# Kernel tuning notes

Hardware: AMD Instinct MI355X
Metric: run time of the kernel (lower is better)

## Reference

```python
import jax, jax.numpy as jnp
import numpy as np
import math

N = 50000      # nodes
E = 800000     # edges
IN = 256       # in_dim
HD = 128       # n_hid
T = 3          # num_types
R = 4          # num_relations
NH = 8         # n_heads
DK = HD // NH  # d_k = 16
L = 2          # n_layers
MAXT = 240     # RTE max_len


def _rte_table():
    # Faithful to the torch code (including its precedence: (10000**arange)/n_hid/2,
    # which overflows to inf for large indices -> div_term -> 0).
    pos = jnp.arange(MAXT, dtype=jnp.float32)[:, None]
    div = 1.0 / (10000.0 ** jnp.arange(0.0, HD * 2, 2.0, dtype=jnp.float32) / HD / 2.0)
    emb = jnp.zeros((MAXT, HD * 2), jnp.float32)
    emb = emb.at[:, 0::2].set(jnp.sin(pos * div) / math.sqrt(HD))
    emb = emb.at[:, 1::2].set(jnp.cos(pos * div) / math.sqrt(HD))
    return emb


def setup_inputs() -> dict:
    key = jax.random.key(0)
    ks = jax.random.split(key, 20)
    s = 0.02
    inp = {}
    inp["node_feature"] = jax.random.normal(ks[0], (N, IN), jnp.float32)
    inp["node_type"] = jax.random.randint(ks[1], (N,), 0, T)
    inp["edge_time"] = jax.random.randint(ks[2], (E,), 0, MAXT)
    inp["edge_type"] = jax.random.randint(ks[3], (E,), 0, R)
    inp["edge_index"] = jax.random.randint(ks[4], (2, E), 0, N)
    # adapt layer (per node type)
    inp["adapt_W"] = jax.random.normal(ks[5], (T, IN, HD), jnp.float32) * s
    inp["adapt_b"] = jax.random.normal(ks[6], (T, HD), jnp.float32) * s
    # per-layer, per-type linears (stored as [in,out] so y = x @ W + b)
    inp["Wk"] = jax.random.normal(ks[7], (L, T, HD, HD), jnp.float32) * s
    inp["bk"] = jnp.zeros((L, T, HD), jnp.float32)
    inp["Wq"] = jax.random.normal(ks[8], (L, T, HD, HD), jnp.float32) * s
    inp["bq"] = jnp.zeros((L, T, HD), jnp.float32)
    inp["Wv"] = jax.random.normal(ks[9], (L, T, HD, HD), jnp.float32) * s
    inp["bv"] = jnp.zeros((L, T, HD), jnp.float32)
    inp["Wa"] = jax.random.normal(ks[10], (L, T, HD, HD), jnp.float32) * s
    inp["ba"] = jnp.zeros((L, T, HD), jnp.float32)
    inp["rel_pri"] = jnp.ones((L, T, R, T, NH), jnp.float32)
    glorot = math.sqrt(6.0 / (DK + DK))
    inp["rel_att"] = jax.random.uniform(ks[11], (L, R, NH, DK, DK), jnp.float32, -glorot, glorot)
    inp["rel_msg"] = jax.random.uniform(ks[12], (L, R, NH, DK, DK), jnp.float32, -glorot, glorot)
    inp["skip"] = jnp.ones((L, T), jnp.float32)
    inp["rte_emb"] = _rte_table()                                   # [240, 2*HD], frozen sinusoid
    inp["rte_W"] = jax.random.normal(ks[13], (L, HD * 2, HD), jnp.float32) * s
    inp["rte_b"] = jnp.zeros((L, HD), jnp.float32)
    return inp


def _per_type_linear(x, types, W, b):
    # x:[M,in], types:[M] in [0,T); W:[T,in,out], b:[T,out]
    out = jnp.zeros((x.shape[0], W.shape[-1]), x.dtype)
    for t in range(W.shape[0]):
        out = jnp.where((types == t)[:, None], x @ W[t] + b[t], out)
    return out


def _segment_softmax(s, seg, n):
    # s:[E,H] softmax over edges sharing the same target node
    m = jax.ops.segment_max(s, seg, num_segments=n)
    e = jnp.exp(s - m[seg])
    z = jax.ops.segment_sum(e, seg, num_segments=n)
    return e / z[seg]


def _forward(node_feature, node_type, edge_time, edge_type, edge_index,
             adapt_W, adapt_b, Wk, bk, Wq, bq, Wv, bv, Wa, ba,
             rel_pri, rel_att, rel_msg, skip, rte_emb, rte_W, rte_b):
    src = edge_index[0]  # j (source)
    dst = edge_index[1]  # i (target)
    st = node_type[src]
    tt = node_type[dst]
    rel1h = jax.nn.one_hot(edge_type, R, dtype=node_feature.dtype)  # [E,R]

    x = jnp.tanh(_per_type_linear(node_feature, node_type, adapt_W, adapt_b))  # [N,HD]

    for l in range(L):
        # relative temporal encoding of source features (per edge)
        rte = rte_emb[edge_time] @ rte_W[l] + rte_b[l]          # [E,HD]
        src_vec = x[src] + rte                                   # [E,HD]
        # q is a pure function of target node features -> compute per node, gather
        q_nodes = _per_type_linear(x, node_type, Wq[l], bq[l])   # [N,HD]
        q = q_nodes[dst].reshape(E, NH, DK)
        k = _per_type_linear(src_vec, st, Wk[l], bk[l]).reshape(E, NH, DK)
        v = _per_type_linear(src_vec, st, Wv[l], bv[l]).reshape(E, NH, DK)
        k = jnp.einsum('ehd,er,rhdk->ehk', k, rel1h, rel_att[l])
        v = jnp.einsum('ehd,er,rhdk->ehk', v, rel1h, rel_msg[l])
        pri = rel_pri[l][tt, edge_type, st]                      # [E,NH]
        score = (q * k).sum(-1) * pri / math.sqrt(DK)            # [E,NH]
        att = _segment_softmax(score, dst, N)                    # [E,NH]
        msg = (v * att[..., None]).reshape(E, HD)                # [E,HD]
        aggr = jax.ops.segment_sum(msg, dst, num_segments=N)     # [N,HD]
        aggr = jax.nn.gelu(aggr, approximate=False)
        out = _per_type_linear(aggr, node_type, Wa[l], ba[l])    # [N,HD]
        alpha = jax.nn.sigmoid(skip[l])[node_type][:, None]      # [N,1]
        x = out * alpha + x * (1.0 - alpha)
    return x


def reference(node_feature, node_type, edge_time, edge_type, edge_index,
              adapt_W, adapt_b, Wk, bk, Wq, bq, Wv, bv, Wa, ba,
              rel_pri, rel_att, rel_msg, skip, rte_emb, rte_W, rte_b):
    return _forward(node_feature, node_type, edge_time, edge_type, edge_index,
                    adapt_W, adapt_b, Wk, bk, Wq, bq, Wv, bv, Wa, ba,
                    rel_pri, rel_att, rel_msg, skip, rte_emb, rte_W, rte_b)
```

## Files before the change

kernel.cpp:

```cpp
#include <hip/hip_runtime.h>
#include <cstdint>
#include <cstddef>


namespace {

constexpr int T_N  = 3;
constexpr int R_N  = 4;
constexpr int HD   = 128;
constexpr int IND  = 256;
constexpr int NH   = 8;
constexpr int MAXT = 240;

typedef unsigned short u16;
typedef unsigned int   u32;
typedef _Float16 f16;
typedef __attribute__((ext_vector_type(8))) _Float16 f16x8;
typedef __attribute__((ext_vector_type(4))) float    f32x4;

__global__ void k_fill_i32(int* __restrict__ p, int v, int n) {
  int i = blockIdx.x * 256 + threadIdx.x;
  if (i < n) p[i] = v;
}
__global__ void k_copy_i32(int* __restrict__ d, const int* __restrict__ s, int n) {
  int i = blockIdx.x * 256 + threadIdx.x;
  if (i < n) d[i] = s[i];
}
__global__ void k_hist_dst(const int* __restrict__ dst, int* __restrict__ cnt, int E) {
  int i = blockIdx.x * 256 + threadIdx.x;
  if (i < E) atomicAdd(&cnt[dst[i]], 1);
}
__global__ void k_scan_a(const int* __restrict__ in, int* __restrict__ out,
                         int* __restrict__ bsums, int n) {
  __shared__ int s[256];
  int gid = blockIdx.x * 256 + threadIdx.x;
  int v = (gid < n) ? in[gid] : 0;
  s[threadIdx.x] = v;
  __syncthreads();
  for (int off = 1; off < 256; off <<= 1) {
    int t = (threadIdx.x >= off) ? s[threadIdx.x - off] : 0;
    __syncthreads();
    s[threadIdx.x] += t;
    __syncthreads();
  }
  if (gid < n) out[gid] = s[threadIdx.x] - v;
  if (threadIdx.x == 255) bsums[blockIdx.x] = s[255];
}
__global__ void k_scan_b(int* __restrict__ bsums, int nb) {
  __shared__ int s[256];
  int v = (threadIdx.x < nb) ? bsums[threadIdx.x] : 0;
  s[threadIdx.x] = v;
  __syncthreads();
  for (int off = 1; off < 256; off <<= 1) {
    int t = (threadIdx.x >= off) ? s[threadIdx.x - off] : 0;
    __syncthreads();
    s[threadIdx.x] += t;
    __syncthreads();
  }
  if (threadIdx.x < nb) bsums[threadIdx.x] = s[threadIdx.x] - v;
}
__global__ void k_scan_c(int* __restrict__ out, const int* __restrict__ bsums, int n) {
  int gid = blockIdx.x * 256 + threadIdx.x;
  if (gid < n) out[gid] += bsums[blockIdx.x];
}
__global__ void k_rank_dst(const int* __restrict__ dst, int* __restrict__ cur,
                           int* __restrict__ rank, int E) {
  int i = blockIdx.x * 256 + threadIdx.x;
  if (i < E) rank[i] = atomicAdd(&cur[dst[i]], 1);
}
__global__ void k_bhist(const int* __restrict__ src, const int* __restrict__ etype,
                        const int* __restrict__ ntype, int* __restrict__ bcnt, int E) {
  __shared__ int loc[12];
  if (threadIdx.x < 12) loc[threadIdx.x] = 0;
  __syncthreads();
  int i = blockIdx.x * 256 + threadIdx.x;
  if (i < E) {
    int b = ntype[src[i]] * R_N + etype[i];
    atomicAdd(&loc[b], 1);
  }
  __syncthreads();
  if (threadIdx.x < 12) atomicAdd(&bcnt[threadIdx.x], loc[threadIdx.x]);
}
__global__ void k_bscan(const int* __restrict__ bcnt, int* __restrict__ bal,
                        int* __restrict__ bcur) {
  if (threadIdx.x == 0 && blockIdx.x == 0) {
    int run = 0;
    for (int b = 0; b < 12; b++) {
      bal[b] = run;
      bcur[b] = run;
      run += (bcnt[b] + 63) & ~63;
    }
    bal[12] = run;
  }
}
__global__ void k_bscatter(const int* __restrict__ src, const int* __restrict__ etype,
                           const int* __restrict__ ntype, int* __restrict__ bcur,
                           int* __restrict__ esorted, int E) {
  __shared__ int loc[12];
  __shared__ int base[12];
  if (threadIdx.x < 12) loc[threadIdx.x] = 0;
  __syncthreads();
  int i = blockIdx.x * 256 + threadIdx.x;
  int b = 0, lpos = 0;
  if (i < E) {
    b = ntype[src[i]] * R_N + etype[i];
    lpos = atomicAdd(&loc[b], 1);
  }
  __syncthreads();
  if (threadIdx.x < 12) {
    int c = loc[threadIdx.x];
    base[threadIdx.x] = (c > 0) ? atomicAdd(&bcur[threadIdx.x], c) : 0;
  }
  __syncthreads();
  if (i < E) esorted[base[b] + lpos] = i;
}
__global__ void k_nhist(const int* __restrict__ ntype, int* __restrict__ ncnt, int N) {
  __shared__ int loc[3];
  if (threadIdx.x < 3) loc[threadIdx.x] = 0;
  __syncthreads();
  int i = blockIdx.x * 256 + threadIdx.x;
  if (i < N) atomicAdd(&loc[ntype[i]], 1);
  __syncthreads();
  if (threadIdx.x < 3) atomicAdd(&ncnt[threadIdx.x], loc[threadIdx.x]);
}
__global__ void k_nscan(const int* __restrict__ ncnt, int* __restrict__ nal,
                        int* __restrict__ ncur) {
  if (threadIdx.x == 0 && blockIdx.x == 0) {
    int run = 0;
    for (int t = 0; t < 3; t++) {
      nal[t] = run;
      ncur[t] = run;
      run += (ncnt[t] + 63) & ~63;
    }
    nal[3] = run;
  }
}
__global__ void k_nscatter(const int* __restrict__ ntype, int* __restrict__ ncur,
                           int* __restrict__ nsorted, int N) {
  __shared__ int loc[3];
  __shared__ int base[3];
  if (threadIdx.x < 3) loc[threadIdx.x] = 0;
  __syncthreads();
  int i = blockIdx.x * 256 + threadIdx.x;
  int t = 0, lpos = 0;
  if (i < N) {
    t = ntype[i];
    lpos = atomicAdd(&loc[t], 1);
  }
  __syncthreads();
  if (threadIdx.x < 3) {
    int c = loc[threadIdx.x];
    base[threadIdx.x] = (c > 0) ? atomicAdd(&ncur[threadIdx.x], c) : 0;
  }
  __syncthreads();
  if (i < N) nsorted[base[t] + lpos] = i;
}

__global__ void k_transp(const float* __restrict__ src, u16* __restrict__ dst,
                         int Kd, int Cd) {
  int c = blockIdx.x;
  int t = blockIdx.y;
  for (int k = threadIdx.x; k < Kd; k += blockDim.x)
    dst[((size_t)t * Cd + c) * Kd + k] =
        __builtin_bit_cast(u16, (f16)src[((size_t)t * Kd + k) * Cd + c]);
}

__global__ void k_rte(const float* __restrict__ emb, const float* __restrict__ W,
                      const float* __restrict__ bias, u16* __restrict__ out, int l) {
  int t = blockIdx.x;
  int lane = threadIdx.x;
  __shared__ __align__(16) float s[2 * HD];
  ((float4*)s)[lane] = ((const float4*)(emb + (size_t)t * 2 * HD))[lane];
  __syncthreads();
  const float* Wl = W + (size_t)l * 2 * HD * HD;
  float o0 = bias[l * HD + 2 * lane];
  float o1 = bias[l * HD + 2 * lane + 1];
  #pragma unroll 4
  for (int k = 0; k < 2 * HD; k++) {
    float xv = s[k];
    float2 w = ((const float2*)(Wl + (size_t)k * HD))[lane];
    o0 = fmaf(xv, w.x, o0);
    o1 = fmaf(xv, w.y, o1);
  }
  u32 pk = (u32)__builtin_bit_cast(u16, (f16)o0)
         | ((u32)__builtin_bit_cast(u16, (f16)o1) << 16);
  ((u32*)out)[t * 64 + lane] = pk;
}

__global__ void k_wcomb(const float* __restrict__ Wk, const float* __restrict__ Wv,
                        const float* __restrict__ bk, const float* __restrict__ bv,
                        const float* __restrict__ Ratt, const float* __restrict__ Rmsg,
                        u16* __restrict__ Wcomb, float* __restrict__ bcomb, int l) {
  int bc = blockIdx.x;
  int b  = bc >> 8;
  int c  = bc & 255;
  int st = b >> 2, rt = b & 3;
  int k  = threadIdx.x;
  bool isv = (c >= HD);
  int c0 = isv ? c - HD : c;
  int h  = c0 >> 4, cc = c0 & 15;
  const float* W = (isv ? Wv : Wk) + (((size_t)(l * T_N + st) * HD) + k) * HD + h * 16;
  const float* A = (isv ? Rmsg : Ratt) + (((size_t)(l * R_N + rt) * NH + h) * 16) * 16 + cc;
  float s = 0.f;
  #pragma unroll
  for (int d = 0; d < 16; d++) s = fmaf(W[d], A[d * 16], s);
  Wcomb[((size_t)b * 256 + c) * HD + k] = __builtin_bit_cast(u16, (f16)s);
  if (k == 0) {
    const float* bb = (isv ? bv : bk) + (size_t)(l * T_N + st) * HD + h * 16;
    float sb = 0.f;
    #pragma unroll
    for (int d = 0; d < 16; d++) sb = fmaf(bb[d], A[d * 16], sb);
    bcomb[b * 256 + c] = sb;
  }
}

template<int K, int ACT, bool AHALF>
__global__ __launch_bounds__(256) void k_ngemm(
    const float* __restrict__ Af, const u16* __restrict__ Ah,
    const u16* __restrict__ WT, const float* __restrict__ bias,
    const int* __restrict__ nsorted, const int* __restrict__ nal,
    const float* __restrict__ skip_l,
    float* __restrict__ out_f, u16* __restrict__ out_h,
    const float* __restrict__ xin) {
  int tile0 = blockIdx.x * 64;
  if (tile0 >= nal[3]) return;
  int t = 0;
  #pragma unroll
  for (int i = 1; i < 3; i++) t += (tile0 >= nal[i]);

  __shared__ __align__(16) u16 ab[64 * K];
  __shared__ int s_nid[64];
  int tid = threadIdx.x;
  int lane = tid & 63, w = tid >> 6;
  int l15 = lane & 15, l4 = lane >> 4;

  if (tid < 64) s_nid[tid] = nsorted[tile0 + tid];
  __syncthreads();

  {
    int r = tid >> 2, q4 = tid & 3;
    int nid = s_nid[r];
    char* rowp = (char*)ab + r * (2 * K);
    int sw = (r & 7) << 4;
    int base = q4 * (K / 2);
    if (nid >= 0) {
      if (AHALF) {
        const f16x8* ap = (const f16x8*)(Ah + (size_t)nid * K + q4 * (K / 4));
        #pragma unroll
        for (int i = 0; i < K / 32; i++)
          *(f16x8*)(rowp + ((base + 16 * i) ^ sw)) = ap[i];
      } else {
        const float4* ap = (const float4*)(Af + (size_t)nid * K + q4 * (K / 4));
        #pragma unroll
        for (int i = 0; i < K / 32; i++) {
          float4 a = ap[2 * i], a2 = ap[2 * i + 1];
          f16x8 hv;
          hv[0] = (f16)a.x;  hv[1] = (f16)a.y;  hv[2] = (f16)a.z;  hv[3] = (f16)a.w;
          hv[4] = (f16)a2.x; hv[5] = (f16)a2.y; hv[6] = (f16)a2.z; hv[7] = (f16)a2.w;
          *(f16x8*)(rowp + ((base + 16 * i) ^ sw)) = hv;
        }
      }
    } else {
      f16x8 z;
      #pragma unroll
      for (int j = 0; j < 8; j++) z[j] = (f16)0.f;
      #pragma unroll
      for (int i = 0; i < K / 32; i++)
        *(f16x8*)(rowp + ((base + 16 * i) ^ sw)) = z;
    }
  }
  __syncthreads();

  f32x4 acc[4][2];
  #pragma unroll
  for (int ni = 0; ni < 2; ni++) {
    float bc = bias[t * HD + w * 32 + ni * 16 + l15];
    #pragma unroll
    for (int mi = 0; mi < 4; mi++) {
      acc[mi][ni][0] = bc; acc[mi][ni][1] = bc;
      acc[mi][ni][2] = bc; acc[mi][ni][3] = bc;
    }
  }
  const u16* Wt = WT + (size_t)t * HD * K;
  #pragma unroll
  for (int ks = 0; ks < K / 32; ks++) {
    int k0 = ks * 32 + 8 * l4;
    f16x8 bf[2], af[4];
    #pragma unroll
    for (int ni = 0; ni < 2; ni++)
      bf[ni] = *(const f16x8*)(Wt + (size_t)(w * 32 + ni * 16 + l15) * K + k0);
    #pragma unroll
    for (int mi = 0; mi < 4; mi++) {
      int row = mi * 16 + l15;
      af[mi] = *(const f16x8*)((const char*)ab + row * (2 * K) +
                               ((2 * k0) ^ ((row & 7) << 4)));
    }
    #pragma unroll
    for (int mi = 0; mi < 4; mi++)
      #pragma unroll
      for (int ni = 0; ni < 2; ni++)
        acc[mi][ni] = __builtin_amdgcn_mfma_f32_16x16x32_f16(af[mi], bf[ni],
                                                             acc[mi][ni], 0, 0, 0);
  }

  float alpha = 0.f;
  if (ACT == 2) alpha = 1.f / (1.f + expf(-skip_l[t]));
  #pragma unroll
  for (int mi = 0; mi < 4; mi++)
    #pragma unroll
    for (int r = 0; r < 4; r++) {
      int rowl = mi * 16 + l4 * 4 + r;
      int nid = s_nid[rowl];
      if (nid >= 0) {
        #pragma unroll
        for (int ni = 0; ni < 2; ni++) {
          int c = w * 32 + ni * 16 + l15;
          float val = acc[mi][ni][r];
          if (ACT == 0) val = tanhf(val);
          if (ACT == 2) {
            float xo = xin[(size_t)nid * HD + c];
            val = val * alpha + xo * (1.f - alpha);
          }
          if (out_f) out_f[(size_t)nid * HD + c] = val;
          if (out_h) out_h[(size_t)nid * HD + c] =
              __builtin_bit_cast(u16, (f16)val);
        }
      }
    }
}

__global__ __launch_bounds__(512) void k_edge_gemm(
    const u16* __restrict__ x_h, const u16* __restrict__ rte_h,
    const u16* __restrict__ Wcomb, const float* __restrict__ bcomb,
    const u16* __restrict__ q_h, const int* __restrict__ esorted,
    const int* __restrict__ bal, const int* __restrict__ src,
    const int* __restrict__ dst, const int* __restrict__ etime,
    const int* __restrict__ ntype, const int* __restrict__ rank,
    const float* __restrict__ pri_l,
    u16* __restrict__ score_h, u16* __restrict__ v_csr) {
  int tile0 = blockIdx.x * 64;
  if (tile0 >= bal[12]) return;
  int b = 0;
  #pragma unroll
  for (int i = 1; i < 12; i++) b += (tile0 >= bal[i]);
  int st = b >> 2, rt = b & 3;

  __shared__ __align__(16) u16 albuf[64 * HD];
  __shared__ int s_eid[64];
  __shared__ int s_dst[64];
  __shared__ int s_rank[64];
  int tid = threadIdx.x;
  int lane = tid & 63, w = tid >> 6;
  int l15 = lane & 15, l4 = lane >> 4;

  if (tid < 64) {
    int e = esorted[tile0 + tid];
    s_eid[tid] = e;
    s_dst[tid] = (e >= 0) ? dst[e] : 0;
    s_rank[tid] = (e >= 0) ? rank[e] : 0;
  }
  __syncthreads();

  {
    int r = tid >> 3, p = tid & 7;
    int e = s_eid[r];
    char* rowp = (char*)albuf + r * 256;
    int sw = (r & 7) << 4;
    if (e >= 0) {
      const f16x8* xs = (const f16x8*)(x_h + (size_t)src[e] * HD + p * 16);
      const f16x8* rp = (const f16x8*)(rte_h + (size_t)etime[e] * HD + p * 16);
      f16x8 h0 = xs[0] + rp[0];
      f16x8 h1 = xs[1] + rp[1];
      *(f16x8*)(rowp + ((p * 32) ^ sw))      = h0;
      *(f16x8*)(rowp + ((p * 32 + 16) ^ sw)) = h1;
    } else {
      f16x8 z;
      #pragma unroll
      for (int j = 0; j < 8; j++) z[j] = (f16)0.f;
      *(f16x8*)(rowp + ((p * 32) ^ sw))      = z;
      *(f16x8*)(rowp + ((p * 32 + 16) ^ sw)) = z;
    }
  }
  __syncthreads();

  f32x4 acc[4][2];
  #pragma unroll
  for (int ni = 0; ni < 2; ni++) {
    float bc = bcomb[b * 256 + w * 32 + ni * 16 + l15];
    #pragma unroll
    for (int mi = 0; mi < 4; mi++) {
      acc[mi][ni][0] = bc; acc[mi][ni][1] = bc;
      acc[mi][ni][2] = bc; acc[mi][ni][3] = bc;
    }
  }
  const u16* Wb = Wcomb + (size_t)b * 256 * HD;
  #pragma unroll
  for (int ks = 0; ks < 4; ks++) {
    int k0 = ks * 32 + 8 * l4;
    f16x8 bf[2], af[4];
    #pragma unroll
    for (int ni = 0; ni < 2; ni++)
      bf[ni] = *(const f16x8*)(Wb + (size_t)(w * 32 + ni * 16 + l15) * HD + k0);
    #pragma unroll
    for (int mi = 0; mi < 4; mi++) {
      int row = mi * 16 + l15;
      af[mi] = *(const f16x8*)((const char*)albuf + row * 256 +
                               ((2 * k0) ^ ((row & 7) << 4)));
    }
    #pragma unroll
    for (int mi = 0; mi < 4; mi++)
      #pragma unroll
      for (int ni = 0; ni < 2; ni++)
        acc[mi][ni] = __builtin_amdgcn_mfma_f32_16x16x32_f16(af[mi], bf[ni],
                                                             acc[mi][ni], 0, 0, 0);
  }
  __syncthreads();

  if (w < 4) {
    #pragma unroll
    for (int mi = 0; mi < 4; mi++)
      #pragma unroll
      for (int r = 0; r < 4; r++) {
        int row = mi * 16 + l4 * 4 + r;
        char* rowp = (char*)albuf + row * 256;
        int sw = (row & 7) << 4;
        #pragma unroll
        for (int ni = 0; ni < 2; ni++) {
          int c = w * 32 + ni * 16 + l15;
          *(u16*)(rowp + ((2 * c) ^ sw)) =
              __builtin_bit_cast(u16, (f16)acc[mi][ni][r]);
        }
      }
  } else {
    int wv = w - 4;
    #pragma unroll
    for (int mi = 0; mi < 4; mi++)
      #pragma unroll
      for (int r = 0; r < 4; r++) {
        int rowl = mi * 16 + l4 * 4 + r;
        if (s_eid[rowl] >= 0) {
          u16* vp = v_csr + (size_t)s_rank[rowl] * HD + wv * 32 + l15;
          #pragma unroll
          for (int ni = 0; ni < 2; ni++)
            vp[ni * 16] = __builtin_bit_cast(u16, (f16)acc[mi][ni][r]);
        }
      }
  }
  __syncthreads();

  {
    int e = tid >> 3, h = tid & 7;
    if (s_eid[e] >= 0) {
      int d = s_dst[e];
      int tt = ntype[d];
      const char* rowp = (const char*)albuf + e * 256;
      int sw = (e & 7) << 4;
      f16x8 kh0 = *(const f16x8*)(rowp + ((h * 32) ^ sw));
      f16x8 kh1 = *(const f16x8*)(rowp + ((h * 32 + 16) ^ sw));
      const f16x8* qp = (const f16x8*)(q_h + (size_t)d * HD + h * 16);
      f16x8 qa = qp[0], qb = qp[1];
      float sc = 0.f;
      #pragma unroll
      for (int j = 0; j < 8; j++) sc += (float)qa[j] * (float)kh0[j];
      #pragma unroll
      for (int j = 0; j < 8; j++) sc += (float)qb[j] * (float)kh1[j];
      float pri = pri_l[((tt * R_N + rt) * T_N + st) * NH + h];
      score_h[(size_t)s_rank[e] * NH + h] =
          __builtin_bit_cast(u16, (f16)(sc * pri * 0.25f));
    }
  }
}

__global__ void k_aggr(const int* __restrict__ row_ptr,
                       const u16* __restrict__ score_h,
                       const u16* __restrict__ v_csr,
                       u16* __restrict__ g_h, int N) {
  int n = blockIdx.x;
  int lane = threadIdx.x;
  int start = row_ptr[n], end = row_ptr[n + 1];

  int h = lane & 7, jj = lane >> 3;
  float m = -3.0e38f;
  for (int idx = start + jj; idx < end; idx += 8)
    m = fmaxf(m, (float)__builtin_bit_cast(f16, score_h[(size_t)idx * NH + h]));
  #pragma unroll
  for (int off = 8; off < 64; off <<= 1) m = fmaxf(m, __shfl_xor(m, off));
  float z = 0.f;
  for (int idx = start + jj; idx < end; idx += 8)
    z += expf((float)__builtin_bit_cast(f16, score_h[(size_t)idx * NH + h]) - m);
  #pragma unroll
  for (int off = 8; off < 64; off <<= 1) z += __shfl_xor(z, off);

  int myh = lane >> 3;
  float md = __shfl(m, myh);
  float zd = __shfl(z, myh);
  float rz = (zd > 0.f) ? 1.f / zd : 0.f;

  float a0 = 0.f, a1 = 0.f;
  for (int idx = start; idx < end; idx++) {
    float sc = (float)__builtin_bit_cast(f16, score_h[(size_t)idx * NH + myh]);
    float wgt = expf(sc - md) * rz;
    u32 v2 = ((const u32*)(v_csr + (size_t)idx * HD))[lane];
    float v0 = (float)__builtin_bit_cast(f16, (u16)(v2 & 0xffffu));
    float v1 = (float)__builtin_bit_cast(f16, (u16)(v2 >> 16));
    a0 = fmaf(wgt, v0, a0);
    a1 = fmaf(wgt, v1, a1);
  }

  a0 = 0.5f * a0 * (1.f + erff(a0 * 0.7071067811865475f));
  a1 = 0.5f * a1 * (1.f + erff(a1 * 0.7071067811865475f));
  u32 pk = (u32)__builtin_bit_cast(u16, (f16)a0)
         | ((u32)__builtin_bit_cast(u16, (f16)a1) << 16);
  ((u32*)(g_h + (size_t)n * HD))[lane] = pk;
}

}

extern "C" void kernel_launch(void* const* d_in, const int* in_sizes, int n_in,
                              void* d_out, int out_size, void* d_ws, size_t ws_size,
                              hipStream_t stream) {
  const float* node_feature = (const float*)d_in[0];
  const int*   node_type    = (const int*)d_in[1];
  const int*   edge_time    = (const int*)d_in[2];
  const int*   edge_type    = (const int*)d_in[3];
  const int*   edge_index   = (const int*)d_in[4];
  const float* adapt_W      = (const float*)d_in[5];
  const float* adapt_b      = (const float*)d_in[6];
  const float* Wk           = (const float*)d_in[7];
  const float* bk           = (const float*)d_in[8];
  const float* Wq           = (const float*)d_in[9];
  const float* bq           = (const float*)d_in[10];
  const float* Wv           = (const float*)d_in[11];
  const float* bv           = (const float*)d_in[12];
  const float* Wa           = (const float*)d_in[13];
  const float* ba           = (const float*)d_in[14];
  const float* rel_pri      = (const float*)d_in[15];
  const float* rel_att      = (const float*)d_in[16];
  const float* rel_msg      = (const float*)d_in[17];
  const float* skip         = (const float*)d_in[18];
  const float* rte_emb      = (const float*)d_in[19];
  const float* rte_W        = (const float*)d_in[20];
  const float* rte_b        = (const float*)d_in[21];

  const int N = in_sizes[1];
  const int E = in_sizes[2];
  const int* src  = edge_index;
  const int* dstp = edge_index + E;

  float* x = (float*)d_out;

  size_t off = 0;
  auto carve = [&](size_t bytes) -> void* {
    void* p = (char*)d_ws + off;
    off += (bytes + 255) & ~(size_t)255;
    return p;
  };
  u16*   v_csr   = (u16*)  carve((size_t)E * HD * 2);
  u16*   score_h = (u16*)  carve((size_t)E * NH * 2);
  u16*   x_h     = (u16*)  carve((size_t)N * HD * 2);
  u16*   qg      = (u16*)  carve((size_t)N * HD * 2);
  u16*   rte_h   = (u16*)  carve((size_t)MAXT * HD * 2);
  u16*   Wcomb   = (u16*)  carve((size_t)12 * 256 * HD * 2);
  float* bcomb   = (float*)carve((size_t)12 * 256 * 4);
  u16*   adaptWT = (u16*)  carve((size_t)T_N * HD * IND * 2);
  u16*   WqT     = (u16*)  carve((size_t)2 * T_N * HD * HD * 2);
  u16*   WaT     = (u16*)  carve((size_t)2 * T_N * HD * HD * 2);
  int*   row_ptr = (int*)  carve((size_t)(N + 1) * 4);
  int*   cnt     = (int*)  carve((size_t)(N + 1) * 4);
  int*   rank    = (int*)  carve((size_t)E * 4);
  int*   bsums   = (int*)  carve(1024 * 4);
  int*   bcnt    = (int*)  carve(16 * 4);
  int*   bal     = (int*)  carve(16 * 4);
  int*   bcur    = (int*)  carve(16 * 4);
  int*   ncnt    = (int*)  carve(16 * 4);
  int*   nal     = (int*)  carve(16 * 4);
  int*   ncur    = (int*)  carve(16 * 4);
  const int EP = E + 12 * 64;
  const int NP = N + 3 * 64;
  int*   esorted = (int*)  carve((size_t)EP * 4);
  int*   nsorted = (int*)  carve((size_t)NP * 4);
  (void)ws_size; (void)n_in; (void)out_size;

  const int gE  = (E + 255) / 256;
  const int gN1 = (N + 1 + 255) / 256;
  const int gN  = (N + 255) / 256;
  const int gEP = (EP + 255) / 256;
  const int gNP = (NP + 255) / 256;
  const int etiles = (EP + 63) / 64;
  const int ntiles = (NP + 63) / 64;

  k_fill_i32<<<gN1, 256, 0, stream>>>(cnt, 0, N + 1);
  k_hist_dst<<<gE, 256, 0, stream>>>(dstp, cnt, E);
  k_scan_a<<<gN1, 256, 0, stream>>>(cnt, row_ptr, bsums, N + 1);
  k_scan_b<<<1, 256, 0, stream>>>(bsums, gN1);
  k_scan_c<<<gN1, 256, 0, stream>>>(row_ptr, bsums, N + 1);
  k_copy_i32<<<gN, 256, 0, stream>>>(cnt, row_ptr, N);
  k_rank_dst<<<gE, 256, 0, stream>>>(dstp, cnt, rank, E);

  k_fill_i32<<<1, 256, 0, stream>>>(bcnt, 0, 16);
  k_bhist<<<gE, 256, 0, stream>>>(src, edge_type, node_type, bcnt, E);
  k_bscan<<<1, 64, 0, stream>>>(bcnt, bal, bcur);
  k_fill_i32<<<gEP, 256, 0, stream>>>(esorted, -1, EP);
  k_bscatter<<<gE, 256, 0, stream>>>(src, edge_type, node_type, bcur, esorted, E);

  k_fill_i32<<<1, 256, 0, stream>>>(ncnt, 0, 16);
  k_nhist<<<gN, 256, 0, stream>>>(node_type, ncnt, N);
  k_nscan<<<1, 64, 0, stream>>>(ncnt, nal, ncur);
  k_fill_i32<<<gNP, 256, 0, stream>>>(nsorted, -1, NP);
  k_nscatter<<<gN, 256, 0, stream>>>(node_type, ncur, nsorted, N);

  k_transp<<<dim3(HD, T_N), 128, 0, stream>>>(adapt_W, adaptWT, IND, HD);
  for (int l = 0; l < 2; l++) {
    k_transp<<<dim3(HD, T_N), 128, 0, stream>>>(
        Wq + (size_t)l * T_N * HD * HD, WqT + (size_t)l * T_N * HD * HD, HD, HD);
    k_transp<<<dim3(HD, T_N), 128, 0, stream>>>(
        Wa + (size_t)l * T_N * HD * HD, WaT + (size_t)l * T_N * HD * HD, HD, HD);
  }

  k_ngemm<IND, 0, false><<<ntiles, 256, 0, stream>>>(
      node_feature, nullptr, adaptWT, adapt_b, nsorted, nal, nullptr,
      x, x_h, nullptr);

  for (int l = 0; l < 2; l++) {
    k_rte<<<MAXT, 64, 0, stream>>>(rte_emb, rte_W, rte_b, rte_h, l);
    k_wcomb<<<12 * 256, 128, 0, stream>>>(Wk, Wv, bk, bv, rel_att, rel_msg,
                                          Wcomb, bcomb, l);
    k_ngemm<HD, 1, true><<<ntiles, 256, 0, stream>>>(
        nullptr, x_h, WqT + (size_t)l * T_N * HD * HD, bq + (size_t)l * T_N * HD,
        nsorted, nal, nullptr, nullptr, qg, nullptr);
    k_edge_gemm<<<etiles, 512, 0, stream>>>(x_h, rte_h, Wcomb, bcomb, qg,
                                            esorted, bal, src, dstp, edge_time,
                                            node_type, rank,
                                            rel_pri + (size_t)l * T_N * R_N * T_N * NH,
                                            score_h, v_csr);
    k_aggr<<<N, 64, 0, stream>>>(row_ptr, score_h, v_csr, qg, N);
    k_ngemm<HD, 2, true><<<ntiles, 256, 0, stream>>>(
        nullptr, qg, WaT + (size_t)l * T_N * HD * HD, ba + (size_t)l * T_N * HD,
        nsorted, nal, skip + (size_t)l * T_N, x, x_h, x);
  }
}
```

Baseline: 889.3 us.

## Make edge GEMM persistent with register-prefetched gathers for the next tile

```diff
diff --git a/kernel.cpp b/kernel.cpp
--- a/kernel.cpp
+++ b/kernel.cpp
@@ -338,134 +338,154 @@
     const int* __restrict__ ntype, const int* __restrict__ rank,
     const float* __restrict__ pri_l,
     u16* __restrict__ score_h, u16* __restrict__ v_csr) {
-  int tile0 = blockIdx.x * 64;
-  if (tile0 >= bal[12]) return;
-  int b = 0;
-  #pragma unroll
-  for (int i = 1; i < 12; i++) b += (tile0 >= bal[i]);
-  int st = b >> 2, rt = b & 3;
-
-  __shared__ __align__(16) u16 albuf[64 * HD];
-  __shared__ int s_eid[64];
-  __shared__ int s_dst[64];
-  __shared__ int s_rank[64];
+  int bal12 = bal[12];
+  int ntt = bal12 >> 6;
+  if ((int)blockIdx.x >= ntt) return;
+
+  __shared__ __align__(16) u16 albuf[2][64 * HD];
+  __shared__ int s_rank[2][64];
+
   int tid = threadIdx.x;
   int lane = tid & 63, w = tid >> 6;
   int l15 = lane & 15, l4 = lane >> 4;
-
-  if (tid < 64) {
-    int e = esorted[tile0 + tid];
-    s_eid[tid] = e;
-    s_dst[tid] = (e >= 0) ? dst[e] : 0;
-    s_rank[tid] = (e >= 0) ? rank[e] : 0;
-  }
-  __syncthreads();
-
-  {
-    int r = tid >> 3, p = tid & 7;
-    int e = s_eid[r];
-    char* rowp = (char*)albuf + r * 256;
-    int sw = (r & 7) << 4;
+  int r8 = tid >> 3, h8 = tid & 7;
+
+  f16x8 xs0, xs1, rp0, rp1, qa, qb;
+  int p_en = -1, p_rk = -1, p_tt = 0;
+  f16x8 cqa, cqb;
+  int c_en, c_rk, c_tt;
+
+  auto PREF = [&](int tn, int buf) {
+    p_en = -1;
+    if (tn >= ntt) return;
+    int e = esorted[tn * 64 + r8];
+    p_en = e;
+    int rk = -1;
     if (e >= 0) {
-      const f16x8* xs = (const f16x8*)(x_h + (size_t)src[e] * HD + p * 16);
-      const f16x8* rp = (const f16x8*)(rte_h + (size_t)etime[e] * HD + p * 16);
-      f16x8 h0 = xs[0] + rp[0];
-      f16x8 h1 = xs[1] + rp[1];
-      *(f16x8*)(rowp + ((p * 32) ^ sw))      = h0;
-      *(f16x8*)(rowp + ((p * 32 + 16) ^ sw)) = h1;
+      int sid = src[e];
+      int tim = etime[e];
+      int d   = dst[e];
+      rk   = rank[e];
+      p_tt = ntype[d];
+      const f16x8* xsp = (const f16x8*)(x_h + (size_t)sid * HD + h8 * 16);
+      const f16x8* rpp = (const f16x8*)(rte_h + (size_t)tim * HD + h8 * 16);
+      xs0 = xsp[0]; xs1 = xsp[1];
+      rp0 = rpp[0]; rp1 = rpp[1];
+      const f16x8* qp = (const f16x8*)(q_h + (size_t)d * HD + h8 * 16);
+      qa = qp[0]; qb = qp[1];
+    }
+    p_rk = rk;
+    if (h8 == 0) s_rank[buf][r8] = rk;
+  };
+
+  PREF(blockIdx.x, 0);
+
+  int it = 0;
+  for (int tile = blockIdx.x; tile < ntt; tile += gridDim.x, ++it) {
+    int cur = it & 1;
+    int tile0 = tile * 64;
+    int b = 0;
+    #pragma unroll
+    for (int i = 1; i < 12; i++) b += (tile0 >= bal[i]);
+    int st = b >> 2, rt = b & 3;
+
+    c_en = p_en; c_rk = p_rk; c_tt = p_tt; cqa = qa; cqb = qb;
+    {
+      char* rowp = (char*)albuf[cur] + r8 * 256;
+      int sw = (r8 & 7) << 4;
+      f16x8 h0, h1;
+      if (c_en >= 0) {
+        h0 = xs0 + rp0;
+        h1 = xs1 + rp1;
+      } else {
+        #pragma unroll
+        for (int j = 0; j < 8; j++) { h0[j] = (f16)0.f; h1[j] = (f16)0.f; }
+      }
+      *(f16x8*)(rowp + ((h8 * 32) ^ sw))      = h0;
+      *(f16x8*)(rowp + ((h8 * 32 + 16) ^ sw)) = h1;
+    }
+    __syncthreads();
+
+    PREF(tile + gridDim.x, cur ^ 1);
+
+    f32x4 acc[4][2];
+    #pragma unroll
+    for (int ni = 0; ni < 2; ni++) {
+      float bc = bcomb[b * 256 + w * 32 + ni * 16 + l15];
+      #pragma unroll
+      for (int mi = 0; mi < 4; mi++) {
+        acc[mi][ni][0] = bc; acc[mi][ni][1] = bc;
+        acc[mi][ni][2] = bc; acc[mi][ni][3] = bc;
+      }
+    }
+    const u16* Wb = Wcomb + (size_t)b * 256 * HD;
+    #pragma unroll
+    for (int ks = 0; ks < 4; ks++) {
+      int k0 = ks * 32 + 8 * l4;
+      f16x8 bf[2], af[4];
+      #pragma unroll
+      for (int ni = 0; ni < 2; ni++)
+        bf[ni] = *(const f16x8*)(Wb + (size_t)(w * 32 + ni * 16 + l15) * HD + k0);
+      #pragma unroll
+      for (int mi = 0; mi < 4; mi++) {
+        int row = mi * 16 + l15;
+        af[mi] = *(const f16x8*)((const char*)albuf[cur] + row * 256 +
+                                 ((2 * k0) ^ ((row & 7) << 4)));
+      }
+      #pragma unroll
+      for (int mi = 0; mi < 4; mi++)
+        #pragma unroll
+        for (int ni = 0; ni < 2; ni++)
+          acc[mi][ni] = __builtin_amdgcn_mfma_f32_16x16x32_f16(af[mi], bf[ni],
+                                                               acc[mi][ni], 0, 0, 0);
+    }
+    __syncthreads();
+
+    if (w < 4) {
+      #pragma unroll
+      for (int mi = 0; mi < 4; mi++)
+        #pragma unroll
+        for (int r = 0; r < 4; r++) {
+          int row = mi * 16 + l4 * 4 + r;
+          char* rowp = (char*)albuf[cur] + row * 256;
+          int sw = (row & 7) << 4;
+          #pragma unroll
+          for (int ni = 0; ni < 2; ni++) {
+            int c = w * 32 + ni * 16 + l15;
+            *(u16*)(rowp + ((2 * c) ^ sw)) =
+                __builtin_bit_cast(u16, (f16)acc[mi][ni][r]);
+          }
+        }
     } else {
-      f16x8 z;
-      #pragma unroll
-      for (int j = 0; j < 8; j++) z[j] = (f16)0.f;
-      *(f16x8*)(rowp + ((p * 32) ^ sw))      = z;
-      *(f16x8*)(rowp + ((p * 32 + 16) ^ sw)) = z;
-    }
-  }
-  __syncthreads();
-
-  f32x4 acc[4][2];
-  #pragma unroll
-  for (int ni = 0; ni < 2; ni++) {
-    float bc = bcomb[b * 256 + w * 32 + ni * 16 + l15];
-    #pragma unroll
-    for (int mi = 0; mi < 4; mi++) {
-      acc[mi][ni][0] = bc; acc[mi][ni][1] = bc;
-      acc[mi][ni][2] = bc; acc[mi][ni][3] = bc;
-    }
-  }
-  const u16* Wb = Wcomb + (size_t)b * 256 * HD;
-  #pragma unroll
-  for (int ks = 0; ks < 4; ks++) {
-    int k0 = ks * 32 + 8 * l4;
-    f16x8 bf[2], af[4];
-    #pragma unroll
-    for (int ni = 0; ni < 2; ni++)
-      bf[ni] = *(const f16x8*)(Wb + (size_t)(w * 32 + ni * 16 + l15) * HD + k0);
-    #pragma unroll
-    for (int mi = 0; mi < 4; mi++) {
-      int row = mi * 16 + l15;
-      af[mi] = *(const f16x8*)((const char*)albuf + row * 256 +
-                               ((2 * k0) ^ ((row & 7) << 4)));
-    }
-    #pragma unroll
-    for (int mi = 0; mi < 4; mi++)
-      #pragma unroll
-      for (int ni = 0; ni < 2; ni++)
-        acc[mi][ni] = __builtin_amdgcn_mfma_f32_16x16x32_f16(af[mi], bf[ni],
-                                                             acc[mi][ni], 0, 0, 0);
-  }
-  __syncthreads();
-
-  if (w < 4) {
-    #pragma unroll
-    for (int mi = 0; mi < 4; mi++)
-      #pragma unroll
-      for (int r = 0; r < 4; r++) {
-        int row = mi * 16 + l4 * 4 + r;
-        char* rowp = (char*)albuf + row * 256;
-        int sw = (row & 7) << 4;
+      int wv = w - 4;
+      #pragma unroll
+      for (int mi = 0; mi < 4; mi++)
         #pragma unroll
-        for (int ni = 0; ni < 2; ni++) {
-          int c = w * 32 + ni * 16 + l15;
-          *(u16*)(rowp + ((2 * c) ^ sw)) =
-              __builtin_bit_cast(u16, (f16)acc[mi][ni][r]);
+        for (int r = 0; r < 4; r++) {
+          int rowl = mi * 16 + l4 * 4 + r;
+          int rk = s_rank[cur][rowl];
+          if (rk >= 0) {
+            u16* vp = v_csr + (size_t)rk * HD + wv * 32 + l15;
+            #pragma unroll
+            for (int ni = 0; ni < 2; ni++)
+              vp[ni * 16] = __builtin_bit_cast(u16, (f16)acc[mi][ni][r]);
+          }
         }
-      }
-  } else {
-    int wv = w - 4;
-    #pragma unroll
-    for (int mi = 0; mi < 4; mi++)
-      #pragma unroll
-      for (int r = 0; r < 4; r++) {
-        int rowl = mi * 16 + l4 * 4 + r;
-        if (s_eid[rowl] >= 0) {
-          u16* vp = v_csr + (size_t)s_rank[rowl] * HD + wv * 32 + l15;
-          #pragma unroll
-          for (int ni = 0; ni < 2; ni++)
-            vp[ni * 16] = __builtin_bit_cast(u16, (f16)acc[mi][ni][r]);
-        }
-      }
-  }
-  __syncthreads();
-
-  {
-    int e = tid >> 3, h = tid & 7;
-    if (s_eid[e] >= 0) {
-      int d = s_dst[e];
-      int tt = ntype[d];
-      const char* rowp = (const char*)albuf + e * 256;
-      int sw = (e & 7) << 4;
-      f16x8 kh0 = *(const f16x8*)(rowp + ((h * 32) ^ sw));
-      f16x8 kh1 = *(const f16x8*)(rowp + ((h * 32 + 16) ^ sw));
-      const f16x8* qp = (const f16x8*)(q_h + (size_t)d * HD + h * 16);
-      f16x8 qa = qp[0], qb = qp[1];
+    }
+    __syncthreads();
+
+    if (c_en >= 0) {
+      const char* rowp = (const char*)albuf[cur] + r8 * 256;
+      int sw = (r8 & 7) << 4;
+      f16x8 kh0 = *(const f16x8*)(rowp + ((h8 * 32) ^ sw));
+      f16x8 kh1 = *(const f16x8*)(rowp + ((h8 * 32 + 16) ^ sw));
       float sc = 0.f;
       #pragma unroll
-      for (int j = 0; j < 8; j++) sc += (float)qa[j] * (float)kh0[j];
-      #pragma unroll
-      for (int j = 0; j < 8; j++) sc += (float)qb[j] * (float)kh1[j];
-      float pri = pri_l[((tt * R_N + rt) * T_N + st) * NH + h];
-      score_h[(size_t)s_rank[e] * NH + h] =
+      for (int j = 0; j < 8; j++) sc += (float)cqa[j] * (float)kh0[j];
+      #pragma unroll
+      for (int j = 0; j < 8; j++) sc += (float)cqb[j] * (float)kh1[j];
+      float pri = pri_l[((c_tt * R_N + rt) * T_N + st) * NH + h8];
+      score_h[(size_t)c_rk * NH + h8] =
           __builtin_bit_cast(u16, (f16)(sc * pri * 0.25f));
     }
   }
@@ -588,6 +608,7 @@
   const int gNP = (NP + 255) / 256;
   const int etiles = (EP + 63) / 64;
   const int ntiles = (NP + 63) / 64;
+  const int egrid  = etiles < 1536 ? etiles : 1536;
 
   k_fill_i32<<<gN1, 256, 0, stream>>>(cnt, 0, N + 1);
   k_hist_dst<<<gE, 256, 0, stream>>>(dstp, cnt, E);
@@ -628,11 +649,11 @@
     k_ngemm<HD, 1, true><<<ntiles, 256, 0, stream>>>(
         nullptr, x_h, WqT + (size_t)l * T_N * HD * HD, bq + (size_t)l * T_N * HD,
         nsorted, nal, nullptr, nullptr, qg, nullptr);
-    k_edge_gemm<<<etiles, 512, 0, stream>>>(x_h, rte_h, Wcomb, bcomb, qg,
-                                            esorted, bal, src, dstp, edge_time,
-                                            node_type, rank,
-                                            rel_pri + (size_t)l * T_N * R_N * T_N * NH,
-                                            score_h, v_csr);
+    k_edge_gemm<<<egrid, 512, 0, stream>>>(x_h, rte_h, Wcomb, bcomb, qg,
+                                           esorted, bal, src, dstp, edge_time,
+                                           node_type, rank,
+                                           rel_pri + (size_t)l * T_N * R_N * T_N * NH,
+                                           score_h, v_csr);
     k_aggr<<<N, 64, 0, stream>>>(row_ptr, score_h, v_csr, qg, N);
     k_ngemm<HD, 2, true><<<ntiles, 256, 0, stream>>>(
         nullptr, qg, WaT + (size_t)l * T_N * HD * HD, ba + (size_t)l * T_N * HD,
```

After: 1.052 ms. +18.3%, slower.
